# Kernel optimization log

Hardware: AMD Instinct MI355X
Metric: run time of the kernel (lower is better)

Reference implementation:

```python
import jax, jax.numpy as jnp
import numpy as np

N, B, D, K_IN, P = 64, 256, 1792, 35, 10
EPS = 1e-5


def setup_inputs() -> dict:
    key = jax.random.key(0)
    ks = jax.random.split(key, 8)
    s_tok = 1.0 / np.sqrt(K_IN)
    s_net = 1.0 / np.sqrt(D)
    return {
        "X": jax.random.normal(ks[0], (N, B, D), dtype=jnp.float32),
        "task_id": jax.random.normal(ks[1], (B, K_IN), dtype=jnp.float32),
        # tokens: Linear(35, 10*1792)
        "W_tok": jax.random.uniform(ks[2], (P * D, K_IN), jnp.float32, -s_tok, s_tok),
        "b_tok": jax.random.uniform(ks[3], (P * D,), jnp.float32, -s_tok, s_tok),
        # ptokens: Linear(35, 1792)
        "W_ptok": jax.random.uniform(ks[4], (D, K_IN), jnp.float32, -s_tok, s_tok),
        "b_ptok": jax.random.uniform(ks[5], (D,), jnp.float32, -s_tok, s_tok),
        # LayerNorm(1792)
        "gamma": jnp.ones((D,), jnp.float32),
        "beta": jnp.zeros((D,), jnp.float32),
        # net: Linear(1792, 10)
        "W_net": jax.random.uniform(ks[6], (P, D), jnp.float32, -s_net, s_net),
        "b_net": jax.random.uniform(ks[7], (P,), jnp.float32, -s_net, s_net),
    }


def _layernorm(x, gamma, beta):
    mu = jnp.mean(x, axis=-1, keepdims=True)
    var = jnp.mean(jnp.square(x - mu), axis=-1, keepdims=True)
    return (x - mu) * jax.lax.rsqrt(var + EPS) * gamma + beta


def reference(X, task_id, W_tok, b_tok, W_ptok, b_ptok, gamma, beta, W_net, b_net):
    # ptokens(task_id): (b, D); identical across n, so compute once and broadcast.
    ptok = task_id @ W_ptok.T + b_ptok                       # (b, D)
    task_token = _layernorm(ptok[None, :, :] + X, gamma, beta)  # (n, b, D)
    # net -> sigmoid: per-token mixing weights over P prompts.
    weight = jax.nn.sigmoid(task_token @ W_net.T + b_net)    # (n, b, P)
    # tokens(task_id): (b, P, D); identical across n, broadcast in einsum.
    prompt_bank = (task_id @ W_tok.T + b_tok).reshape(B, P, D)  # (b, P, D)
    prompt = jnp.einsum("nbp,bpd->nbd", weight, prompt_bank)  # (n, b, D)
    return X + prompt
```

## Files before the change

kernel.cpp:

```cpp
#include <hip/hip_runtime.h>
#include <hip/hip_bf16.h>

#define NN 64
#define BB 256
#define DD 1792
#define KK 35
#define PP 10
#define DQ 448
#define GR 8
#define NGRP 28

typedef float fx4 __attribute__((ext_vector_type(4)));

__device__ __forceinline__ float group16_sum_dpp(float x) {
    asm("v_add_f32_dpp %0, %0, %0 row_shr:1 row_mask:0xf bank_mask:0xf bound_ctrl:0" : "+v"(x));
    asm("v_add_f32_dpp %0, %0, %0 row_shr:2 row_mask:0xf bank_mask:0xf bound_ctrl:0" : "+v"(x));
    asm("v_add_f32_dpp %0, %0, %0 row_shr:4 row_mask:0xf bank_mask:0xf bound_ctrl:0" : "+v"(x));
    asm("v_add_f32_dpp %0, %0, %0 row_shr:8 row_mask:0xf bank_mask:0xf bound_ctrl:0" : "+v"(x));
    return x;
}

__global__ void prep_gf(const float* __restrict__ gamma, const float* __restrict__ beta,
                        const float* __restrict__ Wnet, const float* __restrict__ bnet,
                        float* __restrict__ GF, float* __restrict__ SG, float* __restrict__ ZC) {
    const int p = blockIdx.x;
    const int tid = threadIdx.x;
    float sg = 0.f, sb = 0.f;
#pragma unroll
    for (int j = 0; j < 7; ++j) {
        int d = j * 256 + tid;
        float wv = Wnet[p * DD + d];
        float g = gamma[d] * wv;
        GF[p * DD + d] = g;
        sg += g;
        sb += beta[d] * wv;
    }
#pragma unroll
    for (int off = 32; off > 0; off >>= 1) {
        sg += __shfl_xor(sg, off);
        sb += __shfl_xor(sb, off);
    }
    __shared__ float rs[4][2];
    if ((tid & 63) == 0) { rs[tid >> 6][0] = sg; rs[tid >> 6][1] = sb; }
    __syncthreads();
    if (tid == 0) {
        float a = 0.f, c = 0.f;
#pragma unroll
        for (int w = 0; w < 4; ++w) { a += rs[w][0]; c += rs[w][1]; }
        SG[p] = a;
        ZC[p] = c + bnet[p];
    }
}

__global__ void prep_bank(const float* __restrict__ task,
                          const float* __restrict__ Wtok, const float* __restrict__ btok,
                          const float* __restrict__ Wptok, const float* __restrict__ bptok,
                          float* __restrict__ bank, float* __restrict__ ptok) {
    __shared__ float ti[32 * KK];
    const int tid = threadIdx.x;
    const int b0 = blockIdx.y * 32;
    for (int i = tid; i < 32 * KK; i += 256) ti[i] = task[b0 * KK + i];

    const int r = blockIdx.x * 256 + tid;
    const bool isbank = (r < PP * DD);
    const int rr = isbank ? r : (r - PP * DD);
    const float* __restrict__ W = isbank ? Wtok : Wptok;
    const float bias = isbank ? btok[r] : bptok[rr];

    float w[KK];
#pragma unroll
    for (int k = 0; k < KK; ++k) w[k] = W[rr * KK + k];

    __syncthreads();
#pragma unroll 1
    for (int bb = 0; bb < 32; ++bb) {
        float acc = bias;
#pragma unroll
        for (int k = 0; k < KK; ++k) acc = fmaf(ti[bb * KK + k], w[k], acc);
        const int b = b0 + bb;
        if (isbank) bank[b * (PP * DD) + r] = acc;
        else        ptok[b * DD + rr]       = acc;
    }
}

__global__ __launch_bounds__(448, 1) void fused_pipe(
    const float* __restrict__ X, const float* __restrict__ BANK,
    const float* __restrict__ PTOK, const float* __restrict__ GF,
    const float* __restrict__ SG, const float* __restrict__ ZC,
    float* __restrict__ OUT) {
    const int tid = threadIdx.x;
    const int b = blockIdx.x;

    const float4* __restrict__ X4 = (const float4*)X;
    const float4* __restrict__ B4 = (const float4*)BANK;
    const float4* __restrict__ G4 = (const float4*)GF;
    const float4* __restrict__ P4 = (const float4*)PTOK;
    fx4* __restrict__ OO = (fx4*)OUT;

    __shared__ float red[2][GR][NGRP][12];
    __shared__ float wlds[2][GR][PP];

    const float4 ptk = P4[(size_t)b * DQ + tid];
    float4 gf[PP];
#pragma unroll
    for (int p = 0; p < PP; ++p) gf[p] = G4[(size_t)p * DQ + tid];
    float4 bk[PP];
#pragma unroll
    for (int p = 0; p < PP; ++p) bk[p] = B4[((size_t)b * PP + p) * DQ + tid];

    const bool writer = ((tid & 15) == 15);
    const int g16 = tid >> 4;

    float4 x0[GR], x1[GR], x2[GR];

#define BURST(XN, GN)                                                              \
    {                                                                              \
        _Pragma("unroll")                                                          \
        for (int r = 0; r < GR; ++r)                                               \
            XN[r] = X4[((size_t)((GN) * GR + r) * BB + b) * DQ + tid];             \
        __builtin_amdgcn_sched_barrier(0);                                         \
    }

#define BARRIER_RAW()                                                              \
    asm volatile("s_waitcnt lgkmcnt(0)" ::: "memory");                             \
    __builtin_amdgcn_sched_barrier(0);                                             \
    __builtin_amdgcn_s_barrier();                                                  \
    __builtin_amdgcn_sched_barrier(0);

#define PHASE1(XC, RB)                                                             \
    {                                                                              \
        _Pragma("unroll")                                                          \
        for (int r = 0; r < GR; ++r) {                                             \
            float4 t;                                                              \
            t.x = XC[r].x + ptk.x; t.y = XC[r].y + ptk.y;                          \
            t.z = XC[r].z + ptk.z; t.w = XC[r].w + ptk.w;                          \
            float s1 = t.x + t.y + t.z + t.w;                                      \
            float s2 = t.x * t.x;                                                  \
            s2 = fmaf(t.y, t.y, s2); s2 = fmaf(t.z, t.z, s2);                      \
            s2 = fmaf(t.w, t.w, s2);                                               \
            float a[PP];                                                           \
            _Pragma("unroll")                                                      \
            for (int p = 0; p < PP; ++p) {                                         \
                float v = t.x * gf[p].x;                                           \
                v = fmaf(t.y, gf[p].y, v);                                         \
                v = fmaf(t.z, gf[p].z, v);                                         \
                v = fmaf(t.w, gf[p].w, v);                                         \
                a[p] = v;                                                          \
            }                                                                      \
            s1 = group16_sum_dpp(s1);                                              \
            s2 = group16_sum_dpp(s2);                                              \
            _Pragma("unroll")                                                      \
            for (int p = 0; p < PP; ++p) a[p] = group16_sum_dpp(a[p]);             \
            if (writer) {                                                          \
                float4* dst = (float4*)&red[RB][r][g16][0];                        \
                dst[0] = make_float4(s1, s2, a[0], a[1]);                          \
                dst[1] = make_float4(a[2], a[3], a[4], a[5]);                      \
                dst[2] = make_float4(a[6], a[7], a[8], a[9]);                      \
            }                                                                      \
        }                                                                          \
    }

#define FINALIZE(RB)                                                               \
    if (tid < GR * 16) {                                                           \
        const int row = tid >> 4;                                                  \
        const int v = tid & 15;                                                    \
        float f = 0.f;                                                             \
        if (v < 12) {                                                              \
            _Pragma("unroll")                                                      \
            for (int q = 0; q < NGRP; ++q) f += red[RB][row][q][v];                \
        }                                                                          \
        const int bse = (tid & 63) & ~15;                                          \
        const float mu = __shfl(f, bse)     * (1.0f / (float)DD);                  \
        const float ms = __shfl(f, bse + 1) * (1.0f / (float)DD);                  \
        const float istd = rsqrtf(ms - mu * mu + 1e-5f);                           \
        if (v >= 2 && v < 12) {                                                    \
            const int p = v - 2;                                                   \
            const float z = istd * (f - mu * SG[p]) + ZC[p];                       \
            wlds[RB][row][p] = 1.0f / (1.0f + __expf(-z));                         \
        }                                                                          \
    }

#define PHASE2(XC, WB, GN)                                                         \
    {                                                                              \
        _Pragma("unroll")                                                          \
        for (int r = 0; r < GR; ++r) {                                             \
            float4 acc = XC[r];                                                    \
            _Pragma("unroll")                                                      \
            for (int p = 0; p < PP; ++p) {                                         \
                const float wv = wlds[WB][r][p];                                   \
                acc.x = fmaf(wv, bk[p].x, acc.x);                                  \
                acc.y = fmaf(wv, bk[p].y, acc.y);                                  \
                acc.z = fmaf(wv, bk[p].z, acc.z);                                  \
                acc.w = fmaf(wv, bk[p].w, acc.w);                                  \
            }                                                                      \
            fx4 av; av.x = acc.x; av.y = acc.y; av.z = acc.z; av.w = acc.w;        \
            __builtin_nontemporal_store(av,                                        \
                &OO[((size_t)((GN) * GR + r) * BB + b) * DQ + tid]);               \
        }                                                                          \
    }

    BURST(x0, 0)

    BURST(x1, 1) PHASE1(x0, 0) BARRIER_RAW() FINALIZE(0)
    BURST(x2, 2) PHASE1(x1, 1) BARRIER_RAW() FINALIZE(1) PHASE2(x0, 0, 0)
    BURST(x0, 3) PHASE1(x2, 0) BARRIER_RAW() FINALIZE(0) PHASE2(x1, 1, 1)
    BURST(x1, 4) PHASE1(x0, 1) BARRIER_RAW() FINALIZE(1) PHASE2(x2, 0, 2)
    BURST(x2, 5) PHASE1(x1, 0) BARRIER_RAW() FINALIZE(0) PHASE2(x0, 1, 3)
    BURST(x0, 6) PHASE1(x2, 1) BARRIER_RAW() FINALIZE(1) PHASE2(x1, 0, 4)
    BURST(x1, 7) PHASE1(x0, 0) BARRIER_RAW() FINALIZE(0) PHASE2(x2, 1, 5)
    PHASE1(x1, 1) BARRIER_RAW() FINALIZE(1) PHASE2(x0, 0, 6)
    BARRIER_RAW() PHASE2(x1, 1, 7)

#undef PHASE2
#undef FINALIZE
#undef PHASE1
#undef BARRIER_RAW
#undef BURST
}

extern "C" void kernel_launch(void* const* d_in, const int* in_sizes, int n_in,
                              void* d_out, int out_size, void* d_ws, size_t ws_size,
                              hipStream_t stream) {
    const float* X     = (const float*)d_in[0];
    const float* task  = (const float*)d_in[1];
    const float* Wtok  = (const float*)d_in[2];
    const float* btok  = (const float*)d_in[3];
    const float* Wptok = (const float*)d_in[4];
    const float* bptok = (const float*)d_in[5];
    const float* gamma = (const float*)d_in[6];
    const float* beta  = (const float*)d_in[7];
    const float* Wnet  = (const float*)d_in[8];
    const float* bnet  = (const float*)d_in[9];
    float* out = (float*)d_out;

    float* ws = (float*)d_ws;
    float* bank = ws;
    float* ptok = bank + (size_t)BB * PP * DD;
    float* GF   = ptok + (size_t)BB * DD;
    float* SG   = GF + PP * DD;
    float* ZC   = SG + PP;

    prep_gf<<<PP, 256, 0, stream>>>(gamma, beta, Wnet, bnet, GF, SG, ZC);
    prep_bank<<<dim3(77, 8), 256, 0, stream>>>(task, Wtok, btok, Wptok, bptok, bank, ptok);
    fused_pipe<<<BB, 448, 0, stream>>>(X, bank, ptok, GF, SG, ZC, out);
}
```

Baseline: 73.89 us.

## Tile fused kernel over (b,n) blocks and reread X in a second pass

```diff
diff --git a/kernel.cpp b/kernel.cpp
--- a/kernel.cpp
+++ b/kernel.cpp
@@ -7,7 +7,8 @@
 #define KK 35
 #define PP 10
 #define DQ 448
-#define GR 8
+#define TB 8
+#define TN 8
 #define NGRP 28
 
 typedef float fx4 __attribute__((ext_vector_type(4)));
@@ -83,13 +84,14 @@
     }
 }
 
-__global__ __launch_bounds__(448, 1) void fused_pipe(
+__global__ __launch_bounds__(448, 1) void fused_tile(
     const float* __restrict__ X, const float* __restrict__ BANK,
     const float* __restrict__ PTOK, const float* __restrict__ GF,
     const float* __restrict__ SG, const float* __restrict__ ZC,
     float* __restrict__ OUT) {
     const int tid = threadIdx.x;
-    const int b = blockIdx.x;
+    const int b0 = blockIdx.x * TB;
+    const int n0 = blockIdx.y * TN;
 
     const float4* __restrict__ X4 = (const float4*)X;
     const float4* __restrict__ B4 = (const float4*)BANK;
@@ -97,27 +99,26 @@
     const float4* __restrict__ P4 = (const float4*)PTOK;
     fx4* __restrict__ OO = (fx4*)OUT;
 
-    __shared__ float red[2][GR][NGRP][12];
-    __shared__ float wlds[2][GR][PP];
-
-    const float4 ptk = P4[(size_t)b * DQ + tid];
+    __shared__ float red[TB][NGRP][12];
+    __shared__ float wlds[TN][TB][PP];
+
     float4 gf[PP];
 #pragma unroll
     for (int p = 0; p < PP; ++p) gf[p] = G4[(size_t)p * DQ + tid];
-    float4 bk[PP];
-#pragma unroll
-    for (int p = 0; p < PP; ++p) bk[p] = B4[((size_t)b * PP + p) * DQ + tid];
+    float4 pt[TB];
+#pragma unroll
+    for (int r = 0; r < TB; ++r) pt[r] = P4[(size_t)(b0 + r) * DQ + tid];
 
     const bool writer = ((tid & 15) == 15);
     const int g16 = tid >> 4;
 
-    float4 x0[GR], x1[GR], x2[GR];
-
-#define BURST(XN, GN)                                                              \
+    float4 x0[TB], x1[TB];
+
+#define BURST(XN, G)                                                               \
     {                                                                              \
         _Pragma("unroll")                                                          \
-        for (int r = 0; r < GR; ++r)                                               \
-            XN[r] = X4[((size_t)((GN) * GR + r) * BB + b) * DQ + tid];             \
+        for (int r = 0; r < TB; ++r)                                               \
+            XN[r] = X4[((size_t)(n0 + (G)) * BB + b0 + r) * DQ + tid];             \
         __builtin_amdgcn_sched_barrier(0);                                         \
     }
 
@@ -127,13 +128,13 @@
     __builtin_amdgcn_s_barrier();                                                  \
     __builtin_amdgcn_sched_barrier(0);
 
-#define PHASE1(XC, RB)                                                             \
+#define PHASE1(XC)                                                                 \
     {                                                                              \
         _Pragma("unroll")                                                          \
-        for (int r = 0; r < GR; ++r) {                                             \
+        for (int r = 0; r < TB; ++r) {                                             \
             float4 t;                                                              \
-            t.x = XC[r].x + ptk.x; t.y = XC[r].y + ptk.y;                          \
-            t.z = XC[r].z + ptk.z; t.w = XC[r].w + ptk.w;                          \
+            t.x = XC[r].x + pt[r].x; t.y = XC[r].y + pt[r].y;                      \
+            t.z = XC[r].z + pt[r].z; t.w = XC[r].w + pt[r].w;                      \
             float s1 = t.x + t.y + t.z + t.w;                                      \
             float s2 = t.x * t.x;                                                  \
             s2 = fmaf(t.y, t.y, s2); s2 = fmaf(t.z, t.z, s2);                      \
@@ -152,7 +153,7 @@
             _Pragma("unroll")                                                      \
             for (int p = 0; p < PP; ++p) a[p] = group16_sum_dpp(a[p]);             \
             if (writer) {                                                          \
-                float4* dst = (float4*)&red[RB][r][g16][0];                        \
+                float4* dst = (float4*)&red[r][g16][0];                            \
                 dst[0] = make_float4(s1, s2, a[0], a[1]);                          \
                 dst[1] = make_float4(a[2], a[3], a[4], a[5]);                      \
                 dst[2] = make_float4(a[6], a[7], a[8], a[9]);                      \
@@ -160,14 +161,14 @@
         }                                                                          \
     }
 
-#define FINALIZE(RB)                                                               \
-    if (tid < GR * 16) {                                                           \
+#define FINALIZE(G)                                                                \
+    if (tid < TB * 16) {                                                           \
         const int row = tid >> 4;                                                  \
         const int v = tid & 15;                                                    \
         float f = 0.f;                                                             \
         if (v < 12) {                                                              \
             _Pragma("unroll")                                                      \
-            for (int q = 0; q < NGRP; ++q) f += red[RB][row][q][v];                \
+            for (int q = 0; q < NGRP; ++q) f += red[row][q][v];                    \
         }                                                                          \
         const int bse = (tid & 63) & ~15;                                          \
         const float mu = __shfl(f, bse)     * (1.0f / (float)DD);                  \
@@ -176,42 +177,51 @@
         if (v >= 2 && v < 12) {                                                    \
             const int p = v - 2;                                                   \
             const float z = istd * (f - mu * SG[p]) + ZC[p];                       \
-            wlds[RB][row][p] = 1.0f / (1.0f + __expf(-z));                         \
+            wlds[G][row][p] = 1.0f / (1.0f + __expf(-z));                          \
         }                                                                          \
     }
 
-#define PHASE2(XC, WB, GN)                                                         \
-    {                                                                              \
-        _Pragma("unroll")                                                          \
-        for (int r = 0; r < GR; ++r) {                                             \
-            float4 acc = XC[r];                                                    \
-            _Pragma("unroll")                                                      \
-            for (int p = 0; p < PP; ++p) {                                         \
-                const float wv = wlds[WB][r][p];                                   \
-                acc.x = fmaf(wv, bk[p].x, acc.x);                                  \
-                acc.y = fmaf(wv, bk[p].y, acc.y);                                  \
-                acc.z = fmaf(wv, bk[p].z, acc.z);                                  \
-                acc.w = fmaf(wv, bk[p].w, acc.w);                                  \
-            }                                                                      \
-            fx4 av; av.x = acc.x; av.y = acc.y; av.z = acc.z; av.w = acc.w;        \
-            __builtin_nontemporal_store(av,                                        \
-                &OO[((size_t)((GN) * GR + r) * BB + b) * DQ + tid]);               \
-        }                                                                          \
-    }
-
     BURST(x0, 0)
-
-    BURST(x1, 1) PHASE1(x0, 0) BARRIER_RAW() FINALIZE(0)
-    BURST(x2, 2) PHASE1(x1, 1) BARRIER_RAW() FINALIZE(1) PHASE2(x0, 0, 0)
-    BURST(x0, 3) PHASE1(x2, 0) BARRIER_RAW() FINALIZE(0) PHASE2(x1, 1, 1)
-    BURST(x1, 4) PHASE1(x0, 1) BARRIER_RAW() FINALIZE(1) PHASE2(x2, 0, 2)
-    BURST(x2, 5) PHASE1(x1, 0) BARRIER_RAW() FINALIZE(0) PHASE2(x0, 1, 3)
-    BURST(x0, 6) PHASE1(x2, 1) BARRIER_RAW() FINALIZE(1) PHASE2(x1, 0, 4)
-    BURST(x1, 7) PHASE1(x0, 0) BARRIER_RAW() FINALIZE(0) PHASE2(x2, 1, 5)
-    PHASE1(x1, 1) BARRIER_RAW() FINALIZE(1) PHASE2(x0, 0, 6)
-    BARRIER_RAW() PHASE2(x1, 1, 7)
-
-#undef PHASE2
+#pragma unroll
+    for (int g = 0; g < TN; ++g) {
+        if (g + 1 < TN) {
+            if (g & 1) { BURST(x0, g + 1) } else { BURST(x1, g + 1) }
+        }
+        if (g & 1) { PHASE1(x1) } else { PHASE1(x0) }
+        BARRIER_RAW()
+        FINALIZE(g)
+        BARRIER_RAW()
+    }
+
+#pragma unroll 1
+    for (int r = 0; r < TB; ++r) {
+        float4 bk[PP];
+#pragma unroll
+        for (int p = 0; p < PP; ++p)
+            bk[p] = B4[((size_t)(b0 + r) * PP + p) * DQ + tid];
+
+        float4 xv[TN];
+#pragma unroll
+        for (int n = 0; n < TN; ++n)
+            xv[n] = X4[((size_t)(n0 + n) * BB + b0 + r) * DQ + tid];
+
+#pragma unroll
+        for (int n = 0; n < TN; ++n) {
+            float4 acc = xv[n];
+#pragma unroll
+            for (int p = 0; p < PP; ++p) {
+                const float wv = wlds[n][r][p];
+                acc.x = fmaf(wv, bk[p].x, acc.x);
+                acc.y = fmaf(wv, bk[p].y, acc.y);
+                acc.z = fmaf(wv, bk[p].z, acc.z);
+                acc.w = fmaf(wv, bk[p].w, acc.w);
+            }
+            fx4 av; av.x = acc.x; av.y = acc.y; av.z = acc.z; av.w = acc.w;
+            __builtin_nontemporal_store(av,
+                &OO[((size_t)(n0 + n) * BB + b0 + r) * DQ + tid]);
+        }
+    }
+
 #undef FINALIZE
 #undef PHASE1
 #undef BARRIER_RAW
@@ -242,5 +252,5 @@
 
     prep_gf<<<PP, 256, 0, stream>>>(gamma, beta, Wnet, bnet, GF, SG, ZC);
     prep_bank<<<dim3(77, 8), 256, 0, stream>>>(task, Wtok, btok, Wptok, bptok, bank, ptok);
-    fused_pipe<<<BB, 448, 0, stream>>>(X, bank, ptok, GF, SG, ZC, out);
-}
+    fused_tile<<<dim3(BB / TB, NN / TN), 448, 0, stream>>>(X, bank, ptok, GF, SG, ZC, out);
+}
```

After: 102.1 us. 38.2% more time.

## Split each block into two thread teams covering separate halves of n

Applied to the files above, without the earlier changes.

```diff
diff --git a/kernel.cpp b/kernel.cpp
--- a/kernel.cpp
+++ b/kernel.cpp
@@ -9,6 +9,7 @@
 #define DQ 448
 #define GR 8
 #define NGRP 28
+#define NT_THREADS 896
 
 typedef float fx4 __attribute__((ext_vector_type(4)));
 
@@ -83,13 +84,16 @@
     }
 }
 
-__global__ __launch_bounds__(448, 1) void fused_pipe(
+__global__ __launch_bounds__(NT_THREADS, 1) void fused_pipe2(
     const float* __restrict__ X, const float* __restrict__ BANK,
     const float* __restrict__ PTOK, const float* __restrict__ GF,
     const float* __restrict__ SG, const float* __restrict__ ZC,
     float* __restrict__ OUT) {
-    const int tid = threadIdx.x;
-    const int b = blockIdx.x;
+    const int tid  = threadIdx.x;
+    const int team = (tid >= 448) ? 1 : 0;
+    const int ttid = tid - team * 448;
+    const int b    = blockIdx.x;
+    const int nbase = team * 32;
 
     const float4* __restrict__ X4 = (const float4*)X;
     const float4* __restrict__ B4 = (const float4*)BANK;
@@ -97,19 +101,19 @@
     const float4* __restrict__ P4 = (const float4*)PTOK;
     fx4* __restrict__ OO = (fx4*)OUT;
 
-    __shared__ float red[2][GR][NGRP][12];
-    __shared__ float wlds[2][GR][PP];
-
-    const float4 ptk = P4[(size_t)b * DQ + tid];
+    __shared__ float red[2][2][GR][NGRP][12];
+    __shared__ float wlds[2][2][GR][PP];
+
+    const float4 ptk = P4[(size_t)b * DQ + ttid];
     float4 gf[PP];
 #pragma unroll
-    for (int p = 0; p < PP; ++p) gf[p] = G4[(size_t)p * DQ + tid];
+    for (int p = 0; p < PP; ++p) gf[p] = G4[(size_t)p * DQ + ttid];
     float4 bk[PP];
 #pragma unroll
-    for (int p = 0; p < PP; ++p) bk[p] = B4[((size_t)b * PP + p) * DQ + tid];
-
-    const bool writer = ((tid & 15) == 15);
-    const int g16 = tid >> 4;
+    for (int p = 0; p < PP; ++p) bk[p] = B4[((size_t)b * PP + p) * DQ + ttid];
+
+    const bool writer = ((ttid & 15) == 15);
+    const int g16 = ttid >> 4;
 
     float4 x0[GR], x1[GR], x2[GR];
 
@@ -117,7 +121,7 @@
     {                                                                              \
         _Pragma("unroll")                                                          \
         for (int r = 0; r < GR; ++r)                                               \
-            XN[r] = X4[((size_t)((GN) * GR + r) * BB + b) * DQ + tid];             \
+            XN[r] = X4[((size_t)(nbase + (GN) * GR + r) * BB + b) * DQ + ttid];    \
         __builtin_amdgcn_sched_barrier(0);                                         \
     }
 
@@ -152,7 +156,7 @@
             _Pragma("unroll")                                                      \
             for (int p = 0; p < PP; ++p) a[p] = group16_sum_dpp(a[p]);             \
             if (writer) {                                                          \
-                float4* dst = (float4*)&red[RB][r][g16][0];                        \
+                float4* dst = (float4*)&red[team][RB][r][g16][0];                  \
                 dst[0] = make_float4(s1, s2, a[0], a[1]);                          \
                 dst[1] = make_float4(a[2], a[3], a[4], a[5]);                      \
                 dst[2] = make_float4(a[6], a[7], a[8], a[9]);                      \
@@ -161,22 +165,22 @@
     }
 
 #define FINALIZE(RB)                                                               \
-    if (tid < GR * 16) {                                                           \
-        const int row = tid >> 4;                                                  \
-        const int v = tid & 15;                                                    \
+    if (ttid < GR * 16) {                                                          \
+        const int row = ttid >> 4;                                                 \
+        const int v = ttid & 15;                                                   \
         float f = 0.f;                                                             \
         if (v < 12) {                                                              \
             _Pragma("unroll")                                                      \
-            for (int q = 0; q < NGRP; ++q) f += red[RB][row][q][v];                \
-        }                                                                          \
-        const int bse = (tid & 63) & ~15;                                          \
+            for (int q = 0; q < NGRP; ++q) f += red[team][RB][row][q][v];          \
+        }                                                                          \
+        const int bse = (ttid & 63) & ~15;                                         \
         const float mu = __shfl(f, bse)     * (1.0f / (float)DD);                  \
         const float ms = __shfl(f, bse + 1) * (1.0f / (float)DD);                  \
         const float istd = rsqrtf(ms - mu * mu + 1e-5f);                           \
         if (v >= 2 && v < 12) {                                                    \
             const int p = v - 2;                                                   \
             const float z = istd * (f - mu * SG[p]) + ZC[p];                       \
-            wlds[RB][row][p] = 1.0f / (1.0f + __expf(-z));                         \
+            wlds[team][RB][row][p] = 1.0f / (1.0f + __expf(-z));                   \
         }                                                                          \
     }
 
@@ -187,7 +191,7 @@
             float4 acc = XC[r];                                                    \
             _Pragma("unroll")                                                      \
             for (int p = 0; p < PP; ++p) {                                         \
-                const float wv = wlds[WB][r][p];                                   \
+                const float wv = wlds[team][WB][r][p];                             \
                 acc.x = fmaf(wv, bk[p].x, acc.x);                                  \
                 acc.y = fmaf(wv, bk[p].y, acc.y);                                  \
                 acc.z = fmaf(wv, bk[p].z, acc.z);                                  \
@@ -195,7 +199,7 @@
             }                                                                      \
             fx4 av; av.x = acc.x; av.y = acc.y; av.z = acc.z; av.w = acc.w;        \
             __builtin_nontemporal_store(av,                                        \
-                &OO[((size_t)((GN) * GR + r) * BB + b) * DQ + tid]);               \
+                &OO[((size_t)(nbase + (GN) * GR + r) * BB + b) * DQ + ttid]);      \
         }                                                                          \
     }
 
@@ -204,12 +208,8 @@
     BURST(x1, 1) PHASE1(x0, 0) BARRIER_RAW() FINALIZE(0)
     BURST(x2, 2) PHASE1(x1, 1) BARRIER_RAW() FINALIZE(1) PHASE2(x0, 0, 0)
     BURST(x0, 3) PHASE1(x2, 0) BARRIER_RAW() FINALIZE(0) PHASE2(x1, 1, 1)
-    BURST(x1, 4) PHASE1(x0, 1) BARRIER_RAW() FINALIZE(1) PHASE2(x2, 0, 2)
-    BURST(x2, 5) PHASE1(x1, 0) BARRIER_RAW() FINALIZE(0) PHASE2(x0, 1, 3)
-    BURST(x0, 6) PHASE1(x2, 1) BARRIER_RAW() FINALIZE(1) PHASE2(x1, 0, 4)
-    BURST(x1, 7) PHASE1(x0, 0) BARRIER_RAW() FINALIZE(0) PHASE2(x2, 1, 5)
-    PHASE1(x1, 1) BARRIER_RAW() FINALIZE(1) PHASE2(x0, 0, 6)
-    BARRIER_RAW() PHASE2(x1, 1, 7)
+    PHASE1(x0, 1) BARRIER_RAW() FINALIZE(1) PHASE2(x2, 0, 2)
+    BARRIER_RAW() PHASE2(x0, 1, 3)
 
 #undef PHASE2
 #undef FINALIZE
@@ -242,5 +242,5 @@
 
     prep_gf<<<PP, 256, 0, stream>>>(gamma, beta, Wnet, bnet, GF, SG, ZC);
     prep_bank<<<dim3(77, 8), 256, 0, stream>>>(task, Wtok, btok, Wptok, bptok, bank, ptok);
-    fused_pipe<<<BB, 448, 0, stream>>>(X, bank, ptok, GF, SG, ZC, out);
-}
+    fused_pipe2<<<BB, NT_THREADS, 0, stream>>>(X, bank, ptok, GF, SG, ZC, out);
+}
```

New measurement: 169.0 us. +128.7%, slower.

## Stream gf/bank vectors per group instead of holding them in registers

Applied to the files above, without the earlier changes.

```diff
diff --git a/kernel.cpp b/kernel.cpp
--- a/kernel.cpp
+++ b/kernel.cpp
@@ -7,7 +7,7 @@
 #define KK 35
 #define PP 10
 #define DQ 448
-#define GR 8
+#define GR 4
 #define NGRP 28
 
 typedef float fx4 __attribute__((ext_vector_type(4)));
@@ -83,7 +83,7 @@
     }
 }
 
-__global__ __launch_bounds__(448, 1) void fused_pipe(
+__global__ __launch_bounds__(448, 1) void fused_amort(
     const float* __restrict__ X, const float* __restrict__ BANK,
     const float* __restrict__ PTOK, const float* __restrict__ GF,
     const float* __restrict__ SG, const float* __restrict__ ZC,
@@ -101,23 +101,19 @@
     __shared__ float wlds[2][GR][PP];
 
     const float4 ptk = P4[(size_t)b * DQ + tid];
-    float4 gf[PP];
-#pragma unroll
-    for (int p = 0; p < PP; ++p) gf[p] = G4[(size_t)p * DQ + tid];
-    float4 bk[PP];
-#pragma unroll
-    for (int p = 0; p < PP; ++p) bk[p] = B4[((size_t)b * PP + p) * DQ + tid];
 
     const bool writer = ((tid & 15) == 15);
     const int g16 = tid >> 4;
-
-    float4 x0[GR], x1[GR], x2[GR];
+    const size_t rowstr = (size_t)BB * DQ;
+    const size_t base = (size_t)b * DQ + tid;
+
+    float4 xa[GR], xb[GR];
 
 #define BURST(XN, GN)                                                              \
     {                                                                              \
         _Pragma("unroll")                                                          \
         for (int r = 0; r < GR; ++r)                                               \
-            XN[r] = X4[((size_t)((GN) * GR + r) * BB + b) * DQ + tid];             \
+            XN[r] = X4[(size_t)((GN) * GR + r) * rowstr + base];                   \
         __builtin_amdgcn_sched_barrier(0);                                         \
     }
 
@@ -131,31 +127,42 @@
     {                                                                              \
         _Pragma("unroll")                                                          \
         for (int r = 0; r < GR; ++r) {                                             \
-            float4 t;                                                              \
-            t.x = XC[r].x + ptk.x; t.y = XC[r].y + ptk.y;                          \
-            t.z = XC[r].z + ptk.z; t.w = XC[r].w + ptk.w;                          \
-            float s1 = t.x + t.y + t.z + t.w;                                      \
-            float s2 = t.x * t.x;                                                  \
-            s2 = fmaf(t.y, t.y, s2); s2 = fmaf(t.z, t.z, s2);                      \
-            s2 = fmaf(t.w, t.w, s2);                                               \
-            float a[PP];                                                           \
-            _Pragma("unroll")                                                      \
-            for (int p = 0; p < PP; ++p) {                                         \
-                float v = t.x * gf[p].x;                                           \
-                v = fmaf(t.y, gf[p].y, v);                                         \
-                v = fmaf(t.z, gf[p].z, v);                                         \
-                v = fmaf(t.w, gf[p].w, v);                                         \
-                a[p] = v;                                                          \
+            XC[r].x += ptk.x; XC[r].y += ptk.y;                                    \
+            XC[r].z += ptk.z; XC[r].w += ptk.w;                                    \
+        }                                                                          \
+        float s1[GR], s2[GR], a[GR][PP];                                           \
+        _Pragma("unroll")                                                          \
+        for (int r = 0; r < GR; ++r) {                                             \
+            s1[r] = XC[r].x + XC[r].y + XC[r].z + XC[r].w;                         \
+            float q = XC[r].x * XC[r].x;                                           \
+            q = fmaf(XC[r].y, XC[r].y, q);                                         \
+            q = fmaf(XC[r].z, XC[r].z, q);                                         \
+            q = fmaf(XC[r].w, XC[r].w, q);                                         \
+            s2[r] = q;                                                             \
+        }                                                                          \
+        _Pragma("unroll")                                                          \
+        for (int p = 0; p < PP; ++p) {                                             \
+            const float4 gfp = G4[(size_t)p * DQ + tid];                           \
+            _Pragma("unroll")                                                      \
+            for (int r = 0; r < GR; ++r) {                                         \
+                float v = XC[r].x * gfp.x;                                         \
+                v = fmaf(XC[r].y, gfp.y, v);                                       \
+                v = fmaf(XC[r].z, gfp.z, v);                                       \
+                v = fmaf(XC[r].w, gfp.w, v);                                       \
+                a[r][p] = v;                                                       \
             }                                                                      \
-            s1 = group16_sum_dpp(s1);                                              \
-            s2 = group16_sum_dpp(s2);                                              \
-            _Pragma("unroll")                                                      \
-            for (int p = 0; p < PP; ++p) a[p] = group16_sum_dpp(a[p]);             \
+        }                                                                          \
+        _Pragma("unroll")                                                          \
+        for (int r = 0; r < GR; ++r) {                                             \
+            s1[r] = group16_sum_dpp(s1[r]);                                        \
+            s2[r] = group16_sum_dpp(s2[r]);                                        \
+            _Pragma("unroll")                                                      \
+            for (int p = 0; p < PP; ++p) a[r][p] = group16_sum_dpp(a[r][p]);       \
             if (writer) {                                                          \
                 float4* dst = (float4*)&red[RB][r][g16][0];                        \
-                dst[0] = make_float4(s1, s2, a[0], a[1]);                          \
-                dst[1] = make_float4(a[2], a[3], a[4], a[5]);                      \
-                dst[2] = make_float4(a[6], a[7], a[8], a[9]);                      \
+                dst[0] = make_float4(s1[r], s2[r], a[r][0], a[r][1]);              \
+                dst[1] = make_float4(a[r][2], a[r][3], a[r][4], a[r][5]);          \
+                dst[2] = make_float4(a[r][6], a[r][7], a[r][8], a[r][9]);          \
             }                                                                      \
         }                                                                          \
     }
@@ -182,34 +189,48 @@
 
 #define PHASE2(XC, WB, GN)                                                         \
     {                                                                              \
-        _Pragma("unroll")                                                          \
-        for (int r = 0; r < GR; ++r) {                                             \
-            float4 acc = XC[r];                                                    \
-            _Pragma("unroll")                                                      \
-            for (int p = 0; p < PP; ++p) {                                         \
+        fx4 acc[GR];                                                               \
+        _Pragma("unroll")                                                          \
+        for (int r = 0; r < GR; ++r) {                                             \
+            acc[r].x = XC[r].x - ptk.x; acc[r].y = XC[r].y - ptk.y;                \
+            acc[r].z = XC[r].z - ptk.z; acc[r].w = XC[r].w - ptk.w;                \
+        }                                                                          \
+        _Pragma("unroll")                                                          \
+        for (int p = 0; p < PP; ++p) {                                             \
+            const float4 bkp = B4[((size_t)b * PP + p) * DQ + tid];                \
+            _Pragma("unroll")                                                      \
+            for (int r = 0; r < GR; ++r) {                                         \
                 const float wv = wlds[WB][r][p];                                   \
-                acc.x = fmaf(wv, bk[p].x, acc.x);                                  \
-                acc.y = fmaf(wv, bk[p].y, acc.y);                                  \
-                acc.z = fmaf(wv, bk[p].z, acc.z);                                  \
-                acc.w = fmaf(wv, bk[p].w, acc.w);                                  \
+                acc[r].x = fmaf(wv, bkp.x, acc[r].x);                              \
+                acc[r].y = fmaf(wv, bkp.y, acc[r].y);                              \
+                acc[r].z = fmaf(wv, bkp.z, acc[r].z);                              \
+                acc[r].w = fmaf(wv, bkp.w, acc[r].w);                              \
             }                                                                      \
-            fx4 av; av.x = acc.x; av.y = acc.y; av.z = acc.z; av.w = acc.w;        \
-            __builtin_nontemporal_store(av,                                        \
-                &OO[((size_t)((GN) * GR + r) * BB + b) * DQ + tid]);               \
-        }                                                                          \
-    }
-
-    BURST(x0, 0)
-
-    BURST(x1, 1) PHASE1(x0, 0) BARRIER_RAW() FINALIZE(0)
-    BURST(x2, 2) PHASE1(x1, 1) BARRIER_RAW() FINALIZE(1) PHASE2(x0, 0, 0)
-    BURST(x0, 3) PHASE1(x2, 0) BARRIER_RAW() FINALIZE(0) PHASE2(x1, 1, 1)
-    BURST(x1, 4) PHASE1(x0, 1) BARRIER_RAW() FINALIZE(1) PHASE2(x2, 0, 2)
-    BURST(x2, 5) PHASE1(x1, 0) BARRIER_RAW() FINALIZE(0) PHASE2(x0, 1, 3)
-    BURST(x0, 6) PHASE1(x2, 1) BARRIER_RAW() FINALIZE(1) PHASE2(x1, 0, 4)
-    BURST(x1, 7) PHASE1(x0, 0) BARRIER_RAW() FINALIZE(0) PHASE2(x2, 1, 5)
-    PHASE1(x1, 1) BARRIER_RAW() FINALIZE(1) PHASE2(x0, 0, 6)
-    BARRIER_RAW() PHASE2(x1, 1, 7)
+        }                                                                          \
+        _Pragma("unroll")                                                          \
+        for (int r = 0; r < GR; ++r)                                               \
+            __builtin_nontemporal_store(acc[r],                                    \
+                &OO[(size_t)((GN) * GR + r) * rowstr + base]);                     \
+    }
+
+    BURST(xa, 0)
+
+#pragma unroll 1
+    for (int gp = 0; gp < 8; ++gp) {
+        const int ge = 2 * gp;
+        BURST(xb, ge + 1)
+        PHASE1(xa, 0)
+        BARRIER_RAW()
+        FINALIZE(0)
+        BARRIER_RAW()
+        PHASE2(xa, 0, ge)
+        if (gp < 7) BURST(xa, ge + 2)
+        PHASE1(xb, 1)
+        BARRIER_RAW()
+        FINALIZE(1)
+        BARRIER_RAW()
+        PHASE2(xb, 1, ge + 1)
+    }
 
 #undef PHASE2
 #undef FINALIZE
@@ -242,5 +263,5 @@
 
     prep_gf<<<PP, 256, 0, stream>>>(gamma, beta, Wnet, bnet, GF, SG, ZC);
     prep_bank<<<dim3(77, 8), 256, 0, stream>>>(task, Wtok, btok, Wptok, bptok, bank, ptok);
-    fused_pipe<<<BB, 448, 0, stream>>>(X, bank, ptok, GF, SG, ZC, out);
-}
+    fused_amort<<<BB, 448, 0, stream>>>(X, bank, ptok, GF, SG, ZC, out);
+}
```

Result: slower. 92.53 us (+25.2%).
